# Kernel tuning notes

Hardware: AMD Instinct MI355X
Metric: run time of the kernel (lower is better)

The kernel has to match this reference:

```python
import jax, jax.numpy as jnp
import numpy as np

D_MODEL = 1024
FEED = 4096
HEADS = 16
EPS = 1e-5


def _ln(x, g, b):
    mu = jnp.mean(x, axis=-1, keepdims=True)
    var = jnp.var(x, axis=-1, keepdims=True)
    return (x - mu) * jax.lax.rsqrt(var + EPS) * g + b


def setup_inputs() -> dict:
    key = jax.random.key(0)
    ks = jax.random.split(key, 8)
    s = 0.02
    return {
        "src": jax.random.normal(ks[0], (8, 512, D_MODEL), jnp.float32),
        "wq": jax.random.normal(ks[1], (D_MODEL, D_MODEL), jnp.float32) * s,
        "bq": jnp.zeros((D_MODEL,), jnp.float32),
        "wk": jax.random.normal(ks[2], (D_MODEL, D_MODEL), jnp.float32) * s,
        "bk": jnp.zeros((D_MODEL,), jnp.float32),
        "wv": jax.random.normal(ks[3], (D_MODEL, D_MODEL), jnp.float32) * s,
        "bv": jnp.zeros((D_MODEL,), jnp.float32),
        "g1": jnp.ones((D_MODEL,), jnp.float32),
        "be1": jnp.zeros((D_MODEL,), jnp.float32),
        "w1": jax.random.normal(ks[4], (D_MODEL, FEED), jnp.float32) * s,
        "b1": jnp.zeros((FEED,), jnp.float32),
        "w2": jax.random.normal(ks[5], (FEED, D_MODEL), jnp.float32) * s,
        "b2": jnp.zeros((D_MODEL,), jnp.float32),
        "g2": jnp.ones((D_MODEL,), jnp.float32),
        "be2": jnp.zeros((D_MODEL,), jnp.float32),
    }


def reference(src, wq, bq, wk, bk, wv, bv, g1, be1, w1, b1, w2, b2, g2, be2):
    bs, seq, d = src.shape
    dk = d // HEADS
    q = src @ wq + bq
    k = src @ wk + bk
    v = src @ wv + bv
    # [B, H, S, dk]
    q = q.reshape(bs, seq, HEADS, dk).transpose(0, 2, 1, 3)
    k = k.reshape(bs, seq, HEADS, dk).transpose(0, 2, 1, 3)
    v = v.reshape(bs, seq, HEADS, dk).transpose(0, 2, 1, 3)
    scores = jnp.einsum('bhqd,bhkd->bhqk', q, k)  # no mask (src_mask unused in original)
    att = jax.nn.softmax(scores / jnp.sqrt(jnp.float32(dk)), axis=-1)
    ctx = jnp.einsum('bhqk,bhkd->bhqd', att, v)
    ctx = ctx.transpose(0, 2, 1, 3).reshape(bs, seq, d)  # concat heads
    x = _ln(ctx + src, g1, be1)
    # FFN (dropout = identity at eval)
    h = jax.nn.relu(x @ w1 + b1)
    y = h @ w2 + b2
    return _ln(y + x, g2, be2)
```

## Files before the change

### kernel.cpp

```cpp
#include <hip/hip_runtime.h>
#include <hip/hip_bf16.h>
#include <stdint.h>

#define DM   1024
#define FF   4096
#define NH   16
#define DK   64
#define SEQ  512
#define NTOK 4096

typedef __attribute__((ext_vector_type(8))) unsigned short ushort8;
typedef __attribute__((ext_vector_type(4))) unsigned short ushort4v;
typedef __attribute__((ext_vector_type(8))) short bf16x8;
typedef __attribute__((ext_vector_type(4))) float f32x4;

__device__ __forceinline__ float bf2f(unsigned short u) {
  union { unsigned int i; float f; } v; v.i = ((unsigned int)u) << 16; return v.f;
}
__device__ __forceinline__ unsigned short f2bf(float f) {
  union { float fl; unsigned int i; } v; v.fl = f;
  v.i += 0x7fffu + ((v.i >> 16) & 1u);
  return (unsigned short)(v.i >> 16);
}

__device__ __forceinline__ void gload16(const unsigned short* g, unsigned short* l) {
  __builtin_amdgcn_global_load_lds(
      (const __attribute__((address_space(1))) unsigned int*)g,
      (__attribute__((address_space(3))) unsigned int*)l, 16, 0, 0);
}

__global__ __launch_bounds__(256)
void prep_kernel(const float* __restrict__ src, unsigned short* __restrict__ srcb,
                 const float* __restrict__ wq, const float* __restrict__ wk,
                 const float* __restrict__ wv, unsigned short* __restrict__ WqkvT,
                 const float* __restrict__ w1, unsigned short* __restrict__ W1T,
                 const float* __restrict__ w2, unsigned short* __restrict__ W2T,
                 const float* __restrict__ bq, const float* __restrict__ bk,
                 const float* __restrict__ bv, float* __restrict__ bqkv) {
  const int z = blockIdx.x;
  const int tid = threadIdx.x;
  if (z < 4096) {
    const long i = ((long)z * 256 + tid) * 4;
    f32x4 v = *(const f32x4*)(src + i);
    ushort4v o;
#pragma unroll
    for (int j = 0; j < 4; j++) o[j] = f2bf(v[j]);
    *(ushort4v*)(srcb + i) = o;
    return;
  }
  if (z >= 15360) {
    const int i = (z - 15360) * 256 + tid;
    if (i < 3072)
      bqkv[i] = (i < 1024) ? bq[i] : ((i < 2048) ? bk[i - 1024] : bv[i - 2048]);
    return;
  }
  const float* in;
  unsigned short* out;
  int ldin, ldout;
  long r0, c0;
  if (z < 7168) {
    const int w = (z - 4096) >> 10;
    const int t = (z - 4096) & 1023;
    in = (w == 0) ? wq : (w == 1) ? wk : wv;
    out = WqkvT + (long)w * 1024 * 1024;
    ldin = 1024; ldout = 1024;
    r0 = (long)(t >> 5) * 32; c0 = (long)(t & 31) * 32;
  } else if (z < 11264) {
    const int t = z - 7168;
    in = w1; out = W1T; ldin = 4096; ldout = 1024;
    r0 = (long)(t >> 7) * 32; c0 = (long)(t & 127) * 32;
  } else {
    const int t = z - 11264;
    in = w2; out = W2T; ldin = 1024; ldout = 4096;
    r0 = (long)(t >> 5) * 32; c0 = (long)(t & 31) * 32;
  }
  __shared__ unsigned short tile[32][33];
  const int tx = tid & 31, ty = tid >> 5;
#pragma unroll
  for (int i = 0; i < 4; i++)
    tile[ty + i * 8][tx] = f2bf(in[(r0 + ty + i * 8) * ldin + c0 + tx]);
  __syncthreads();
#pragma unroll
  for (int i = 0; i < 4; i++)
    out[(c0 + ty + i * 8) * ldout + r0 + tx] = tile[tx][ty + i * 8];
}

template <bool RELU, bool PARTIAL>
__global__ __launch_bounds__(512, 2)
void gemm256(const unsigned short* __restrict__ A, int lda,
             const unsigned short* __restrict__ B, int ldb,
             const float* __restrict__ bias,
             unsigned short* __restrict__ C,
             unsigned short* __restrict__ P1,
             unsigned short* __restrict__ P2,
             unsigned short* __restrict__ P3,
             int ldc, int nTN) {
  __shared__ unsigned short sm[65536];
  const int tid = threadIdx.x;
  const int lane = tid & 63;
  const int wid = tid >> 6;
  const int wr = wid >> 2, wc = wid & 3;
  const int kgrp = wid >> 2;

  const unsigned int T = gridDim.x;
  const unsigned int q8 = T >> 3;
  const unsigned int x = blockIdx.x;
  const unsigned int swz = (x & 7) * q8 + (x >> 3);
  const long bm = (long)(swz / nTN) * 256;
  const long bn = (long)(swz % nTN) * 256;
  const long kbase = (long)blockIdx.y * 1024;

  f32x4 acc[8][4];
#pragma unroll
  for (int mf = 0; mf < 8; mf++)
#pragma unroll
    for (int nf = 0; nf < 4; nf++) acc[mf][nf] = f32x4{0.f, 0.f, 0.f, 0.f};

  const int strow = tid >> 2;
  const int scol = (((tid & 3) ^ ((tid >> 3) & 3)) << 3);
  const unsigned short* pA = A + (bm + strow) * lda + kbase + scol;
  const unsigned short* pB = B + (bn + strow) * ldb + kbase + scol;
  unsigned short* dA = sm + tid * 8;
  unsigned short* dB = sm + 32768 + tid * 8;

  const int g = lane >> 4;
  int offA[8], offB[4];
#pragma unroll
  for (int mf = 0; mf < 8; mf++) {
    const int rm = wr * 128 + mf * 16 + (lane & 15);
    offA[mf] = rm * 32 + ((g ^ ((rm >> 1) & 3)) << 3);
  }
#pragma unroll
  for (int nf = 0; nf < 4; nf++) {
    const int rb = wc * 64 + nf * 16 + (lane & 15);
    offB[nf] = rb * 32 + ((g ^ ((rb >> 1) & 3)) << 3);
  }

#define GA(kt, ks, rh, bu) gload16(pA + (long)(rh) * 128 * lda + (kt) * 64 + (ks) * 32, \
                                   dA + (bu) * 16384 + (ks) * 8192 + (rh) * 4096)
#define GB(kt, ks, rh, bu) gload16(pB + (long)(rh) * 128 * ldb + (kt) * 64 + (ks) * 32, \
                                   dB + (bu) * 16384 + (ks) * 8192 + (rh) * 4096)
#define MF16(AR, BR, MO)                                                      \
  do {                                                                        \
    __builtin_amdgcn_s_setprio(1);                                            \
    _Pragma("unroll")                                                         \
    for (int mf = 0; mf < 4; mf++)                                            \
      _Pragma("unroll")                                                       \
      for (int nf = 0; nf < 4; nf++)                                          \
        acc[(MO) + mf][nf] = __builtin_amdgcn_mfma_f32_16x16x32_bf16(         \
            AR[mf], BR[nf], acc[(MO) + mf][nf], 0, 0, 0);                     \
    __builtin_amdgcn_s_setprio(0);                                            \
  } while (0)

  GA(0, 0, 0, 0); GA(0, 0, 1, 0); GA(0, 1, 0, 0); GA(0, 1, 1, 0);
  GB(0, 0, 0, 0); GB(0, 0, 1, 0); GB(0, 1, 0, 0); GB(0, 1, 1, 0);

  for (int t = 0; t < 16; ++t) {
    const int c = t & 1, n2 = c ^ 1;
    const int k1 = t + 1;
    const unsigned short* smAc = sm + c * 16384;
    const unsigned short* smBc = sm + 32768 + c * 16384;
    bf16x8 a_[4], bcur[4];
    const int ks0off = kgrp * 8192;
    const int ks1off = (1 - kgrp) * 8192;

    GA(k1, 0, 0, n2); GA(k1, 0, 1, n2);
    asm volatile("s_waitcnt vmcnt(2)\ns_barrier" ::: "memory");
#pragma unroll
    for (int nf = 0; nf < 4; nf++) bcur[nf] = *(const bf16x8*)(smBc + ks0off + offB[nf]);
#pragma unroll
    for (int mf = 0; mf < 4; mf++) a_[mf] = *(const bf16x8*)(smAc + ks0off + offA[mf]);
    MF16(a_, bcur, 0);
    GA(k1, 1, 0, n2); GA(k1, 1, 1, n2);
#pragma unroll
    for (int mf = 0; mf < 4; mf++) a_[mf] = *(const bf16x8*)(smAc + ks0off + offA[4 + mf]);
    asm volatile("s_barrier" ::: "memory");
    MF16(a_, bcur, 4);
    GB(k1, 0, 0, n2); GB(k1, 0, 1, n2);
#pragma unroll
    for (int nf = 0; nf < 4; nf++) bcur[nf] = *(const bf16x8*)(smBc + ks1off + offB[nf]);
#pragma unroll
    for (int mf = 0; mf < 4; mf++) a_[mf] = *(const bf16x8*)(smAc + ks1off + offA[mf]);
    asm volatile("s_barrier" ::: "memory");
    MF16(a_, bcur, 0);
    GB(k1, 1, 0, n2); GB(k1, 1, 1, n2);
#pragma unroll
    for (int mf = 0; mf < 4; mf++) a_[mf] = *(const bf16x8*)(smAc + ks1off + offA[4 + mf]);
    asm volatile("s_waitcnt lgkmcnt(0)\ns_barrier" ::: "memory");
    MF16(a_, bcur, 4);
  }
#undef GA
#undef GB
#undef MF16

  asm volatile("s_waitcnt vmcnt(0)" ::: "memory");

  unsigned short* Cw = C;
  if (PARTIAL) {
    const int kc = blockIdx.y;
    Cw = (kc == 0) ? C : (kc == 1) ? P1 : (kc == 2) ? P2 : P3;
  }

  __syncthreads();
  {
    const int lrow = wr * 128 + ((lane >> 4) << 2);
    const int lcol = wc * 64 + (lane & 15);
#pragma unroll
    for (int nf = 0; nf < 4; nf++) {
      const int col = lcol + nf * 16;
      const float bv = PARTIAL ? 0.f : bias[bn + col];
#pragma unroll
      for (int mf = 0; mf < 8; mf++) {
#pragma unroll
        for (int i = 0; i < 4; i++) {
          float v = acc[mf][nf][i] + bv;
          if (RELU) v = fmaxf(v, 0.f);
          sm[(lrow + mf * 16 + i) * 256 + col] = f2bf(v);
        }
      }
    }
  }
  __syncthreads();
  const int srow = tid >> 5;
  const int scol8 = (tid & 31) * 8;
#pragma unroll
  for (int p = 0; p < 16; ++p) {
    const int r = p * 16 + srow;
    ushort8 vrow = *(const ushort8*)(sm + r * 256 + scol8);
    *(ushort8*)(&Cw[(bm + r) * ldc + bn + scol8]) = vrow;
  }
}

__global__ __launch_bounds__(512, 2)
void gemm_qkv(const unsigned short* __restrict__ A,
              const unsigned short* __restrict__ B,
              const float* __restrict__ bias,
              unsigned short* __restrict__ C,
              unsigned short* __restrict__ Vt) {
  __shared__ unsigned short sm[65536];
  const int tid = threadIdx.x;
  const int lane = tid & 63;
  const int wid = tid >> 6;

  const unsigned int x = blockIdx.x;
  const unsigned int swz = (x & 7) * 32 + (x >> 3);
  const long bm = (long)(swz >> 3) * 128;
  const long bn = (long)(swz & 7) * 384;

  f32x4 acc[8][3];
#pragma unroll
  for (int mf = 0; mf < 8; mf++)
#pragma unroll
    for (int nf = 0; nf < 3; nf++) acc[mf][nf] = f32x4{0.f, 0.f, 0.f, 0.f};

  const int strow = tid >> 2;
  const int scol = (((tid & 3) ^ ((tid >> 3) & 3)) << 3);
  const unsigned short* pA = A + (bm + strow) * 1024 + scol;
  const unsigned short* pB = B + (bn + strow) * 1024 + scol;
  unsigned short* dA = sm + tid * 8;
  unsigned short* dB = sm + 16384 + tid * 8;

  const int g = lane >> 4;
  int offA[8], offB[3];
#pragma unroll
  for (int mf = 0; mf < 8; mf++) {
    const int rm = mf * 16 + (lane & 15);
    offA[mf] = rm * 32 + ((g ^ ((rm >> 1) & 3)) << 3);
  }
#pragma unroll
  for (int nf = 0; nf < 3; nf++) {
    const int rb = wid * 48 + nf * 16 + (lane & 15);
    offB[nf] = rb * 32 + ((g ^ ((rb >> 1) & 3)) << 3);
  }

#define GAQ(kt, ks, bu) gload16(pA + (kt) * 64 + (ks) * 32,                    \
                                dA + (bu) * 8192 + (ks) * 4096)
#define GBQ(kt, ks, rh, bu) gload16(pB + (long)(rh) * 128 * 1024 + (kt) * 64 + (ks) * 32, \
                                    dB + (bu) * 24576 + (ks) * 12288 + (rh) * 4096)
#define MFQ(AR, MO)                                                           \
  do {                                                                        \
    __builtin_amdgcn_s_setprio(1);                                            \
    _Pragma("unroll")                                                         \
    for (int mf = 0; mf < 4; mf++)                                            \
      _Pragma("unroll")                                                       \
      for (int nf = 0; nf < 3; nf++)                                          \
        acc[(MO) + mf][nf] = __builtin_amdgcn_mfma_f32_16x16x32_bf16(         \
            AR[mf], bcur[nf], acc[(MO) + mf][nf], 0, 0, 0);                   \
    __builtin_amdgcn_s_setprio(0);                                            \
  } while (0)

  GAQ(0, 0, 0); GAQ(0, 1, 0);
  GBQ(0, 0, 0, 0); GBQ(0, 0, 1, 0); GBQ(0, 0, 2, 0);
  GBQ(0, 1, 0, 0); GBQ(0, 1, 1, 0); GBQ(0, 1, 2, 0);

  for (int t = 0; t < 16; ++t) {
    const int c = t & 1, n2 = c ^ 1;
    const int k1 = t + 1;
    const unsigned short* smA = sm + c * 8192;
    const unsigned short* smB = sm + 16384 + c * 24576;
    bf16x8 a_[4], bcur[3];

    GAQ(k1, 0, n2); GAQ(k1, 1, n2);
    asm volatile("s_waitcnt vmcnt(2)\ns_barrier" ::: "memory");
#pragma unroll
    for (int nf = 0; nf < 3; nf++) bcur[nf] = *(const bf16x8*)(smB + offB[nf]);
#pragma unroll
    for (int mf = 0; mf < 4; mf++) a_[mf] = *(const bf16x8*)(smA + offA[mf]);
    MFQ(a_, 0);
    GBQ(k1, 0, 0, n2); GBQ(k1, 0, 1, n2);
#pragma unroll
    for (int mf = 0; mf < 4; mf++) a_[mf] = *(const bf16x8*)(smA + offA[4 + mf]);
    asm volatile("s_barrier" ::: "memory");
    MFQ(a_, 4);
    GBQ(k1, 0, 2, n2); GBQ(k1, 1, 0, n2);
#pragma unroll
    for (int nf = 0; nf < 3; nf++) bcur[nf] = *(const bf16x8*)(smB + 12288 + offB[nf]);
#pragma unroll
    for (int mf = 0; mf < 4; mf++) a_[mf] = *(const bf16x8*)(smA + 4096 + offA[mf]);
    asm volatile("s_barrier" ::: "memory");
    MFQ(a_, 0);
    GBQ(k1, 1, 1, n2); GBQ(k1, 1, 2, n2);
#pragma unroll
    for (int mf = 0; mf < 4; mf++) a_[mf] = *(const bf16x8*)(smA + 4096 + offA[4 + mf]);
    asm volatile("s_waitcnt lgkmcnt(0)\ns_barrier" ::: "memory");
    MFQ(a_, 4);
  }
#undef GAQ
#undef GBQ
#undef MFQ

  asm volatile("s_waitcnt vmcnt(0)" ::: "memory");

  const int bq16 = (int)(bm >> 9) * 16;
  const int s0 = (int)(bm & 511);
  const int lrow = (lane >> 4) << 2;
  const bool anyC = (bn < 2048);
  if (anyC) __syncthreads();

#pragma unroll
  for (int nf = 0; nf < 3; nf++) {
    const int gbase = (int)bn + wid * 48 + nf * 16;
    const float bv = bias[gbase + (lane & 15)];
    if (gbase >= 2048) {
      const int gc = gbase - 2048;
      const int h = gc >> 6;
      const int d = (gc & 63) + (lane & 15);
      unsigned short* vb = Vt + ((long)(bq16 + h) * 64 + d) * 512 + s0 + lrow;
#pragma unroll
      for (int mf = 0; mf < 8; mf++) {
        ushort4v o;
#pragma unroll
        for (int i = 0; i < 4; i++) o[i] = f2bf(acc[mf][nf][i] + bv);
        *(ushort4v*)(vb + mf * 16) = o;
      }
    } else {
      const int lc = wid * 48 + nf * 16 + (lane & 15);
#pragma unroll
      for (int mf = 0; mf < 8; mf++) {
#pragma unroll
        for (int i = 0; i < 4; i++)
          sm[(mf * 16 + lrow + i) * 384 + lc] = f2bf(acc[mf][nf][i] + bv);
      }
    }
  }

  if (anyC) {
    __syncthreads();
    const int r = tid >> 2;
    const int nseg = (bn == 1920) ? 4 : 12;
    for (int p = 0; p < nseg; ++p) {
      const int seg = p * 4 + (tid & 3);
      ushort8 v = *(const ushort8*)(sm + r * 384 + seg * 8);
      *(ushort8*)(&C[(bm + r) * 3072 + bn + seg * 8]) = v;
    }
  }
}

__global__ __launch_bounds__(256)
void attn_kernel(const unsigned short* __restrict__ QKV,
                 const unsigned short* __restrict__ Vt,
                 unsigned short* __restrict__ CTX) {
  const int lin = blockIdx.x;
  const int xcd = lin & 7;
  const int slot = lin >> 3;
  const int bh = xcd + 8 * (slot >> 3);
  const int qt = slot & 7;
  const int b = bh >> 4, h = bh & 15;
  const int tid = threadIdx.x;
  const int lane = tid & 63;
  const int wid = tid >> 6;

  __shared__ unsigned short Ks[64][72];
  __shared__ unsigned short Vs[64][72];
  __shared__ unsigned short Ps[4][16][72];

  const int qrow0 = qt * 64 + wid * 16;
  const unsigned short* Qb = QKV + (long)(b * SEQ + qrow0) * 3072 + h * 64;
  bf16x8 aq[2];
#pragma unroll
  for (int ks = 0; ks < 2; ks++)
    aq[ks] = *(const bf16x8*)(Qb + (long)(lane & 15) * 3072 + ks * 32 +
                              (lane >> 4) * 8);

  f32x4 acc_o[4];
#pragma unroll
  for (int n = 0; n < 4; n++) acc_o[n] = f32x4{0.f, 0.f, 0.f, 0.f};
  float rsum[4] = {0.f, 0.f, 0.f, 0.f};

  const int sr = tid >> 3;
  const int sc = (tid & 7) * 8;
  const unsigned short* Kg = QKV + (long)(b * SEQ) * 3072 + 1024 + h * 64 + sc;
  const unsigned short* Vg = Vt + (long)bh * (DK * SEQ) + sc;

  ushort8 kr0 = *(const ushort8*)(Kg + (long)sr * 3072);
  ushort8 kr1 = *(const ushort8*)(Kg + (long)(sr + 32) * 3072);
  ushort8 vr0 = *(const ushort8*)(Vg + (long)sr * SEQ);
  ushort8 vr1 = *(const ushort8*)(Vg + (long)(sr + 32) * SEQ);

#pragma unroll
  for (int c = 0; c < 8; ++c) {
    __syncthreads();
    *(ushort8*)(&Ks[sr][sc]) = kr0;
    *(ushort8*)(&Ks[sr + 32][sc]) = kr1;
    *(ushort8*)(&Vs[sr][sc]) = vr0;
    *(ushort8*)(&Vs[sr + 32][sc]) = vr1;
    if (c < 7) {
      kr0 = *(const ushort8*)(Kg + (long)((c + 1) * 64 + sr) * 3072);
      kr1 = *(const ushort8*)(Kg + (long)((c + 1) * 64 + sr + 32) * 3072);
      vr0 = *(const ushort8*)(Vg + (long)sr * SEQ + (c + 1) * 64);
      vr1 = *(const ushort8*)(Vg + (long)(sr + 32) * SEQ + (c + 1) * 64);
    }
    __syncthreads();

    f32x4 s[4];
#pragma unroll
    for (int n = 0; n < 4; n++) s[n] = f32x4{0.f, 0.f, 0.f, 0.f};
#pragma unroll
    for (int ks = 0; ks < 2; ks++) {
      bf16x8 kf[4];
#pragma unroll
      for (int n = 0; n < 4; n++)
        kf[n] = *(const bf16x8*)(&Ks[n * 16 + (lane & 15)][ks * 32 + (lane >> 4) * 8]);
#pragma unroll
      for (int n = 0; n < 4; n++)
        s[n] = __builtin_amdgcn_mfma_f32_16x16x32_bf16(aq[ks], kf[n], s[n], 0, 0, 0);
    }

#pragma unroll
    for (int n = 0; n < 4; n++) {
#pragma unroll
      for (int i = 0; i < 4; i++) {
        const float p = __expf(s[n][i] * 0.125f);
        rsum[i] += p;
        Ps[wid][(lane >> 4) * 4 + i][n * 16 + (lane & 15)] = f2bf(p);
      }
    }

#pragma unroll
    for (int ks = 0; ks < 2; ks++) {
      bf16x8 pa = *(const bf16x8*)(&Ps[wid][lane & 15][ks * 32 + (lane >> 4) * 8]);
      bf16x8 vf[4];
#pragma unroll
      for (int n = 0; n < 4; n++)
        vf[n] = *(const bf16x8*)(&Vs[n * 16 + (lane & 15)][ks * 32 + (lane >> 4) * 8]);
#pragma unroll
      for (int n = 0; n < 4; n++)
        acc_o[n] = __builtin_amdgcn_mfma_f32_16x16x32_bf16(pa, vf[n], acc_o[n], 0, 0, 0);
    }
  }

#pragma unroll
  for (int i = 0; i < 4; i++) {
#pragma unroll
    for (int off = 1; off < 16; off <<= 1) rsum[i] += __shfl_xor(rsum[i], off, 64);
  }

  const long orow0 = (long)(b * SEQ + qrow0);
#pragma unroll
  for (int i = 0; i < 4; i++) {
    const float inv = 1.f / rsum[i];
    const long r = orow0 + (lane >> 4) * 4 + i;
#pragma unroll
    for (int n = 0; n < 4; n++)
      CTX[r * DM + h * 64 + n * 16 + (lane & 15)] = f2bf(acc_o[n][i] * inv);
  }
}

__global__ __launch_bounds__(256)
void ln1_kernel(const unsigned short* __restrict__ X,
                const unsigned short* __restrict__ R,
                const float* __restrict__ g,
                const float* __restrict__ be,
                unsigned short* __restrict__ Ob) {
  const int t = blockIdx.x;
  const int tid = threadIdx.x;
  const long base = (long)t * DM + tid * 4;
  __shared__ float red[8];

  ushort4v xv = *(const ushort4v*)(X + base);
  ushort4v rv = *(const ushort4v*)(R + base);
  float v[4];
#pragma unroll
  for (int j = 0; j < 4; j++) v[j] = bf2f(xv[j]) + bf2f(rv[j]);
  float s = v[0] + v[1] + v[2] + v[3];
  float q = v[0] * v[0] + v[1] * v[1] + v[2] * v[2] + v[3] * v[3];
#pragma unroll
  for (int off = 1; off < 64; off <<= 1) {
    s += __shfl_xor(s, off, 64);
    q += __shfl_xor(q, off, 64);
  }
  if ((tid & 63) == 0) { red[tid >> 6] = s; red[4 + (tid >> 6)] = q; }
  __syncthreads();
  s = red[0] + red[1] + red[2] + red[3];
  q = red[4] + red[5] + red[6] + red[7];
  const float mu = s * (1.f / DM);
  const float var = q * (1.f / DM) - mu * mu;
  const float rstd = rsqrtf(fmaxf(var, 0.f) + 1e-5f);

  f32x4 gv = *(const f32x4*)(g + tid * 4);
  f32x4 bv = *(const f32x4*)(be + tid * 4);
  ushort4v ob;
#pragma unroll
  for (int j = 0; j < 4; j++)
    ob[j] = f2bf((v[j] - mu) * rstd * gv[j] + bv[j]);
  *(ushort4v*)(Ob + base) = ob;
}

__global__ __launch_bounds__(256)
void ln2_kernel(const unsigned short* __restrict__ P0,
                const unsigned short* __restrict__ P1,
                const unsigned short* __restrict__ P2,
                const unsigned short* __restrict__ P3,
                const float* __restrict__ b2,
                const unsigned short* __restrict__ R,
                const float* __restrict__ g,
                const float* __restrict__ be,
                float* __restrict__ O) {
  const int t = blockIdx.x;
  const int tid = threadIdx.x;
  const long base = (long)t * DM + tid * 4;
  __shared__ float red[8];

  ushort4v p0 = *(const ushort4v*)(P0 + base);
  ushort4v p1 = *(const ushort4v*)(P1 + base);
  ushort4v p2 = *(const ushort4v*)(P2 + base);
  ushort4v p3 = *(const ushort4v*)(P3 + base);
  f32x4 bb = *(const f32x4*)(b2 + tid * 4);
  ushort4v rv = *(const ushort4v*)(R + base);
  float v[4];
#pragma unroll
  for (int j = 0; j < 4; j++)
    v[j] = bf2f(p0[j]) + bf2f(p1[j]) + bf2f(p2[j]) + bf2f(p3[j]) + bb[j] + bf2f(rv[j]);
  float s = v[0] + v[1] + v[2] + v[3];
  float q = v[0] * v[0] + v[1] * v[1] + v[2] * v[2] + v[3] * v[3];
#pragma unroll
  for (int off = 1; off < 64; off <<= 1) {
    s += __shfl_xor(s, off, 64);
    q += __shfl_xor(q, off, 64);
  }
  if ((tid & 63) == 0) { red[tid >> 6] = s; red[4 + (tid >> 6)] = q; }
  __syncthreads();
  s = red[0] + red[1] + red[2] + red[3];
  q = red[4] + red[5] + red[6] + red[7];
  const float mu = s * (1.f / DM);
  const float var = q * (1.f / DM) - mu * mu;
  const float rstd = rsqrtf(fmaxf(var, 0.f) + 1e-5f);

  f32x4 gv = *(const f32x4*)(g + tid * 4);
  f32x4 bv = *(const f32x4*)(be + tid * 4);
  f32x4 of;
#pragma unroll
  for (int j = 0; j < 4; j++) of[j] = (v[j] - mu) * rstd * gv[j] + bv[j];
  *(f32x4*)(O + base) = of;
}

extern "C" void kernel_launch(void* const* d_in, const int* in_sizes, int n_in,
                              void* d_out, int out_size, void* d_ws, size_t ws_size,
                              hipStream_t stream) {
  const float* src = (const float*)d_in[0];
  const float* wq  = (const float*)d_in[1];
  const float* bq  = (const float*)d_in[2];
  const float* wk  = (const float*)d_in[3];
  const float* bk  = (const float*)d_in[4];
  const float* wv  = (const float*)d_in[5];
  const float* bv  = (const float*)d_in[6];
  const float* g1  = (const float*)d_in[7];
  const float* be1 = (const float*)d_in[8];
  const float* w1  = (const float*)d_in[9];
  const float* b1  = (const float*)d_in[10];
  const float* w2  = (const float*)d_in[11];
  const float* b2  = (const float*)d_in[12];
  const float* g2  = (const float*)d_in[13];
  const float* be2 = (const float*)d_in[14];
  float* out = (float*)d_out;

  char* ws = (char*)d_ws;
  const size_t MB = 1024 * 1024;
  unsigned short* srcb  = (unsigned short*)(ws + 0);
  unsigned short* WqkvT = (unsigned short*)(ws + 8 * MB);
  float*          bqkv  = (float*)(ws + 14 * MB);
  unsigned short* W1T   = (unsigned short*)(ws + 15 * MB);
  unsigned short* W2T   = (unsigned short*)(ws + 23 * MB);
  unsigned short* QKV   = (unsigned short*)(ws + 31 * MB);
  unsigned short* Vtb   = (unsigned short*)(ws + 55 * MB);
  unsigned short* CTX   = (unsigned short*)(ws + 63 * MB);
  unsigned short* X1    = (unsigned short*)(ws + 71 * MB);
  unsigned short* Pk3   = (unsigned short*)(ws + 79 * MB);
  unsigned short* Hb    = (unsigned short*)(ws + 31 * MB);
  unsigned short* Pk0   = (unsigned short*)(ws + 0);
  unsigned short* Pk1   = (unsigned short*)(ws + 15 * MB);
  unsigned short* Pk2   = (unsigned short*)(ws + 63 * MB);
  if (ws_size < 87 * MB) return;

  prep_kernel<<<15372, 256, 0, stream>>>(src, srcb, wq, wk, wv, WqkvT,
                                         w1, W1T, w2, W2T, bq, bk, bv, bqkv);

  gemm_qkv<<<256, 512, 0, stream>>>(srcb, WqkvT, bqkv, QKV, Vtb);
  attn_kernel<<<1024, 256, 0, stream>>>(QKV, Vtb, CTX);
  ln1_kernel<<<NTOK, 256, 0, stream>>>(CTX, srcb, g1, be1, X1);
  gemm256<true, false><<<dim3(256, 1), 512, 0, stream>>>(
      X1, 1024, W1T, 1024, b1, Hb, nullptr, nullptr, nullptr, 4096, 16);
  gemm256<false, true><<<dim3(64, 4), 512, 0, stream>>>(
      Hb, 4096, W2T, 4096, nullptr, Pk0, Pk1, Pk2, Pk3, 1024, 4);
  ln2_kernel<<<NTOK, 256, 0, stream>>>(Pk0, Pk1, Pk2, Pk3, b2, X1, g2, be2, out);
}
```

Baseline: 160.3 us.

## Shrink FFN GEMM tiles to 256x128 with simpler single-stage K loop

The FFN GEMMs now use 256x128 output tiles instead of 256x256. The main loop steps through K in 32-wide slices with a single double-buffered load and MFMA block per iteration, replacing the staggered four-phase schedule. This halves LDS use and accumulator registers and doubles the grid size, so more blocks can be resident on more CUs. In exchange, each tile reuses the data it loads less, and barriers come more often relative to the MFMA work.

```diff
diff --git a/kernel.cpp b/kernel.cpp
--- a/kernel.cpp
+++ b/kernel.cpp
@@ -87,32 +87,31 @@
 
 template <bool RELU, bool PARTIAL>
 __global__ __launch_bounds__(512, 2)
-void gemm256(const unsigned short* __restrict__ A, int lda,
-             const unsigned short* __restrict__ B, int ldb,
-             const float* __restrict__ bias,
-             unsigned short* __restrict__ C,
-             unsigned short* __restrict__ P1,
-             unsigned short* __restrict__ P2,
-             unsigned short* __restrict__ P3,
-             int ldc, int nTN) {
-  __shared__ unsigned short sm[65536];
+void gemm256n(const unsigned short* __restrict__ A, int lda,
+              const unsigned short* __restrict__ B, int ldb,
+              const float* __restrict__ bias,
+              unsigned short* __restrict__ C,
+              unsigned short* __restrict__ P1,
+              unsigned short* __restrict__ P2,
+              unsigned short* __restrict__ P3,
+              int ldc, int nTN) {
+  __shared__ unsigned short sm[32768];
   const int tid = threadIdx.x;
   const int lane = tid & 63;
   const int wid = tid >> 6;
-  const int wr = wid >> 2, wc = wid & 3;
-  const int kgrp = wid >> 2;
+  const int wr = wid >> 1, wc = wid & 1;
 
   const unsigned int T = gridDim.x;
   const unsigned int q8 = T >> 3;
   const unsigned int x = blockIdx.x;
   const unsigned int swz = (x & 7) * q8 + (x >> 3);
   const long bm = (long)(swz / nTN) * 256;
-  const long bn = (long)(swz % nTN) * 256;
+  const long bn = (long)(swz % nTN) * 128;
   const long kbase = (long)blockIdx.y * 1024;
 
-  f32x4 acc[8][4];
-#pragma unroll
-  for (int mf = 0; mf < 8; mf++)
+  f32x4 acc[4][4];
+#pragma unroll
+  for (int mf = 0; mf < 4; mf++)
 #pragma unroll
     for (int nf = 0; nf < 4; nf++) acc[mf][nf] = f32x4{0.f, 0.f, 0.f, 0.f};
 
@@ -121,13 +120,13 @@
   const unsigned short* pA = A + (bm + strow) * lda + kbase + scol;
   const unsigned short* pB = B + (bn + strow) * ldb + kbase + scol;
   unsigned short* dA = sm + tid * 8;
-  unsigned short* dB = sm + 32768 + tid * 8;
+  unsigned short* dB = sm + 16384 + tid * 8;
 
   const int g = lane >> 4;
-  int offA[8], offB[4];
-#pragma unroll
-  for (int mf = 0; mf < 8; mf++) {
-    const int rm = wr * 128 + mf * 16 + (lane & 15);
+  int offA[4], offB[4];
+#pragma unroll
+  for (int mf = 0; mf < 4; mf++) {
+    const int rm = wr * 64 + mf * 16 + (lane & 15);
     offA[mf] = rm * 32 + ((g ^ ((rm >> 1) & 3)) << 3);
   }
 #pragma unroll
@@ -136,62 +135,37 @@
     offB[nf] = rb * 32 + ((g ^ ((rb >> 1) & 3)) << 3);
   }
 
-#define GA(kt, ks, rh, bu) gload16(pA + (long)(rh) * 128 * lda + (kt) * 64 + (ks) * 32, \
-                                   dA + (bu) * 16384 + (ks) * 8192 + (rh) * 4096)
-#define GB(kt, ks, rh, bu) gload16(pB + (long)(rh) * 128 * ldb + (kt) * 64 + (ks) * 32, \
-                                   dB + (bu) * 16384 + (ks) * 8192 + (rh) * 4096)
-#define MF16(AR, BR, MO)                                                      \
-  do {                                                                        \
-    __builtin_amdgcn_s_setprio(1);                                            \
-    _Pragma("unroll")                                                         \
-    for (int mf = 0; mf < 4; mf++)                                            \
-      _Pragma("unroll")                                                       \
-      for (int nf = 0; nf < 4; nf++)                                          \
-        acc[(MO) + mf][nf] = __builtin_amdgcn_mfma_f32_16x16x32_bf16(         \
-            AR[mf], BR[nf], acc[(MO) + mf][nf], 0, 0, 0);                     \
-    __builtin_amdgcn_s_setprio(0);                                            \
-  } while (0)
-
-  GA(0, 0, 0, 0); GA(0, 0, 1, 0); GA(0, 1, 0, 0); GA(0, 1, 1, 0);
-  GB(0, 0, 0, 0); GB(0, 0, 1, 0); GB(0, 1, 0, 0); GB(0, 1, 1, 0);
-
-  for (int t = 0; t < 16; ++t) {
+#define GA2(kt, rh, bu) gload16(pA + (long)(rh) * 128 * lda + (kt) * 32, \
+                                dA + (bu) * 8192 + (rh) * 4096)
+#define GB1(kt, bu)     gload16(pB + (kt) * 32, dB + (bu) * 4096)
+
+  GA2(0, 0, 0); GA2(0, 1, 0); GB1(0, 0);
+
+  for (int t = 0; t < 32; ++t) {
     const int c = t & 1, n2 = c ^ 1;
-    const int k1 = t + 1;
-    const unsigned short* smAc = sm + c * 16384;
-    const unsigned short* smBc = sm + 32768 + c * 16384;
-    bf16x8 a_[4], bcur[4];
-    const int ks0off = kgrp * 8192;
-    const int ks1off = (1 - kgrp) * 8192;
-
-    GA(k1, 0, 0, n2); GA(k1, 0, 1, n2);
-    asm volatile("s_waitcnt vmcnt(2)\ns_barrier" ::: "memory");
-#pragma unroll
-    for (int nf = 0; nf < 4; nf++) bcur[nf] = *(const bf16x8*)(smBc + ks0off + offB[nf]);
-#pragma unroll
-    for (int mf = 0; mf < 4; mf++) a_[mf] = *(const bf16x8*)(smAc + ks0off + offA[mf]);
-    MF16(a_, bcur, 0);
-    GA(k1, 1, 0, n2); GA(k1, 1, 1, n2);
-#pragma unroll
-    for (int mf = 0; mf < 4; mf++) a_[mf] = *(const bf16x8*)(smAc + ks0off + offA[4 + mf]);
-    asm volatile("s_barrier" ::: "memory");
-    MF16(a_, bcur, 4);
-    GB(k1, 0, 0, n2); GB(k1, 0, 1, n2);
-#pragma unroll
-    for (int nf = 0; nf < 4; nf++) bcur[nf] = *(const bf16x8*)(smBc + ks1off + offB[nf]);
-#pragma unroll
-    for (int mf = 0; mf < 4; mf++) a_[mf] = *(const bf16x8*)(smAc + ks1off + offA[mf]);
-    asm volatile("s_barrier" ::: "memory");
-    MF16(a_, bcur, 0);
-    GB(k1, 1, 0, n2); GB(k1, 1, 1, n2);
-#pragma unroll
-    for (int mf = 0; mf < 4; mf++) a_[mf] = *(const bf16x8*)(smAc + ks1off + offA[4 + mf]);
+    const int k1 = (t + 1) & 31;
+    GA2(k1, 0, n2); GA2(k1, 1, n2); GB1(k1, n2);
+    asm volatile("s_waitcnt vmcnt(3)\ns_barrier" ::: "memory");
+
+    const unsigned short* smA = sm + c * 8192;
+    const unsigned short* smB = sm + 16384 + c * 4096;
+    bf16x8 a_[4], b_[4];
+#pragma unroll
+    for (int nf = 0; nf < 4; nf++) b_[nf] = *(const bf16x8*)(smB + offB[nf]);
+#pragma unroll
+    for (int mf = 0; mf < 4; mf++) a_[mf] = *(const bf16x8*)(smA + offA[mf]);
     asm volatile("s_waitcnt lgkmcnt(0)\ns_barrier" ::: "memory");
-    MF16(a_, bcur, 4);
-  }
-#undef GA
-#undef GB
-#undef MF16
+    __builtin_amdgcn_s_setprio(1);
+#pragma unroll
+    for (int mf = 0; mf < 4; mf++)
+#pragma unroll
+      for (int nf = 0; nf < 4; nf++)
+        acc[mf][nf] = __builtin_amdgcn_mfma_f32_16x16x32_bf16(
+            a_[mf], b_[nf], acc[mf][nf], 0, 0, 0);
+    __builtin_amdgcn_s_setprio(0);
+  }
+#undef GA2
+#undef GB1
 
   asm volatile("s_waitcnt vmcnt(0)" ::: "memory");
 
@@ -203,30 +177,30 @@
 
   __syncthreads();
   {
-    const int lrow = wr * 128 + ((lane >> 4) << 2);
+    const int lrow = wr * 64 + ((lane >> 4) << 2);
     const int lcol = wc * 64 + (lane & 15);
 #pragma unroll
     for (int nf = 0; nf < 4; nf++) {
       const int col = lcol + nf * 16;
       const float bv = PARTIAL ? 0.f : bias[bn + col];
 #pragma unroll
-      for (int mf = 0; mf < 8; mf++) {
+      for (int mf = 0; mf < 4; mf++) {
 #pragma unroll
         for (int i = 0; i < 4; i++) {
           float v = acc[mf][nf][i] + bv;
           if (RELU) v = fmaxf(v, 0.f);
-          sm[(lrow + mf * 16 + i) * 256 + col] = f2bf(v);
+          sm[(lrow + mf * 16 + i) * 128 + col] = f2bf(v);
         }
       }
     }
   }
   __syncthreads();
-  const int srow = tid >> 5;
-  const int scol8 = (tid & 31) * 8;
-#pragma unroll
-  for (int p = 0; p < 16; ++p) {
-    const int r = p * 16 + srow;
-    ushort8 vrow = *(const ushort8*)(sm + r * 256 + scol8);
+  const int srow = tid >> 4;
+  const int scol8 = (tid & 15) * 8;
+#pragma unroll
+  for (int p = 0; p < 8; ++p) {
+    const int r = p * 32 + srow;
+    ushort8 vrow = *(const ushort8*)(sm + r * 128 + scol8);
     *(ushort8*)(&Cw[(bm + r) * ldc + bn + scol8]) = vrow;
   }
 }
@@ -618,9 +592,9 @@
   gemm_qkv<<<256, 512, 0, stream>>>(srcb, WqkvT, bqkv, QKV, Vtb);
   attn_kernel<<<1024, 256, 0, stream>>>(QKV, Vtb, CTX);
   ln1_kernel<<<NTOK, 256, 0, stream>>>(CTX, srcb, g1, be1, X1);
-  gemm256<true, false><<<dim3(256, 1), 512, 0, stream>>>(
-      X1, 1024, W1T, 1024, b1, Hb, nullptr, nullptr, nullptr, 4096, 16);
-  gemm256<false, true><<<dim3(64, 4), 512, 0, stream>>>(
-      Hb, 4096, W2T, 4096, nullptr, Pk0, Pk1, Pk2, Pk3, 1024, 4);
+  gemm256n<true, false><<<dim3(512, 1), 512, 0, stream>>>(
+      X1, 1024, W1T, 1024, b1, Hb, nullptr, nullptr, nullptr, 4096, 32);
+  gemm256n<false, true><<<dim3(128, 4), 512, 0, stream>>>(
+      Hb, 4096, W2T, 4096, nullptr, Pk0, Pk1, Pk2, Pk3, 1024, 8);
   ln2_kernel<<<NTOK, 256, 0, stream>>>(Pk0, Pk1, Pk2, Pk3, b2, X1, g2, be2, out);
 }
```

New measurement: 170.8 us. 6.5% more time.
